# Kernel optimization log

Hardware: AMD Instinct MI355X
Metric: run time of the kernel (lower is better)

Reference implementation:

```python
import jax, jax.numpy as jnp
import numpy as np

N, E, ND, ED, HID = 50000, 400000, 128, 64, 128
GIN = 2 * ND + 2  # gnn1 input dim
CIN = 2 * HID + ED  # classifier input dim


def seg_mean(v, idx, n):
    s = jax.ops.segment_sum(v, idx, num_segments=n)
    cnt = jax.ops.segment_sum(jnp.ones((v.shape[0], 1), v.dtype), idx, num_segments=n)
    return s / jnp.maximum(cnt, 1.0)


def layer_norm(h, g, b):
    mu = h.mean(-1, keepdims=True)
    var = ((h - mu) ** 2).mean(-1, keepdims=True)
    return (h - mu) / jnp.sqrt(var + 1e-5) * g + b


def gatv2(h, src, dst, ea, wl, wr, we, att, bias, n, heads):
    # PyG GATv2Conv, concat=False, negative_slope=0.2, add_self_loops with fill_value='mean'
    C = wl.shape[1] // heads
    loop_attr = seg_mean(ea, dst, n)  # self-loop edge_attr = mean of incoming edge_attr
    ar = jnp.arange(n, dtype=src.dtype)
    s = jnp.concatenate([src, ar])
    d = jnp.concatenate([dst, ar])
    ea2 = jnp.concatenate([ea, loop_attr], axis=0)
    xl = (h @ wl).reshape(n, heads, C)
    xr = (h @ wr).reshape(n, heads, C)
    e = xl[s] + xr[d] + (ea2 @ we).reshape(-1, heads, C)  # [E2, H, C]
    e = jax.nn.leaky_relu(e, 0.2)
    logit = (e * att).sum(-1)  # [E2, H]
    m = jax.ops.segment_max(logit, d, num_segments=n)
    m = jnp.where(jnp.isfinite(m), m, 0.0)
    a = jnp.exp(logit - m[d])
    denom = jax.ops.segment_sum(a, d, num_segments=n)
    a = a / jnp.maximum(denom[d], 1e-16)
    out = jax.ops.segment_sum(xl[s] * a[..., None], d, num_segments=n)  # [N, H, C]
    return out.mean(axis=1) + bias


def setup_inputs() -> dict:
    key = jax.random.key(0)
    ks = jax.random.split(key, 32)
    w = lambda k, sh: jax.random.normal(k, sh, jnp.float32) * 0.05
    x = jax.random.normal(ks[0], (N, ND), jnp.float32)
    node_stats = jax.random.uniform(ks[1], (N, 2), jnp.float32)
    src = jax.random.randint(ks[2], (E,), 0, N)
    dst = (src + 1 + jax.random.randint(ks[3], (E,), 0, N - 1)) % N  # guarantees src != dst
    edge_index = jnp.stack([src, dst]).astype(jnp.int32)
    edge_attr = jax.random.normal(ks[4], (E, ED), jnp.float32)
    return {
        'x': x, 'node_stats': node_stats, 'edge_index': edge_index, 'edge_attr': edge_attr,
        'epw': w(ks[5], (ED, ND)), 'epb': jnp.zeros((ND,), jnp.float32),
        'g1wl': w(ks[6], (GIN, 2 * HID)), 'g1wr': w(ks[7], (GIN, 2 * HID)),
        'g1we': w(ks[8], (ED, 2 * HID)), 'g1att': w(ks[9], (2, HID)), 'g1b': jnp.zeros((HID,), jnp.float32),
        'n1g': jnp.ones((HID,), jnp.float32), 'n1b': jnp.zeros((HID,), jnp.float32),
        'g2wl': w(ks[10], (HID, HID)), 'g2wr': w(ks[11], (HID, HID)),
        'g2we': w(ks[12], (ED, HID)), 'g2att': w(ks[13], (1, HID)), 'g2b': jnp.zeros((HID,), jnp.float32),
        'n2g': jnp.ones((HID,), jnp.float32), 'n2b': jnp.zeros((HID,), jnp.float32),
        'c1w': w(ks[14], (CIN, HID)), 'c1b': jnp.zeros((HID,), jnp.float32),
        'c2w': w(ks[15], (HID, HID // 2)), 'c2b': jnp.zeros((HID // 2,), jnp.float32),
        'c3w': w(ks[16], (HID // 2, 1)), 'c3b': jnp.zeros((1,), jnp.float32),
    }


def reference(x, node_stats, edge_index, edge_attr, epw, epb, g1wl, g1wr, g1we, g1att, g1b,
              n1g, n1b, g2wl, g2wr, g2we, g2att, g2b, n2g, n2b, c1w, c1b, c2w, c2b, c3w, c3b):
    src, dst = edge_index[0], edge_index[1]
    n = x.shape[0]
    emb = jax.nn.relu(edge_attr @ epw + epb)  # [E, ND]
    x_out = seg_mean(emb, src, n)
    x_in = seg_mean(emb, dst, n)
    xi = jnp.concatenate([x_out, x_in, node_stats], axis=1)  # [N, GIN]
    h1 = jax.nn.elu(layer_norm(gatv2(xi, src, dst, edge_attr, g1wl, g1wr, g1we, g1att, g1b, n, 2), n1g, n1b))
    h2 = jax.nn.elu(layer_norm(gatv2(h1, src, dst, edge_attr, g2wl, g2wr, g2we, g2att, g2b, n, 1), n2g, n2b))
    er = jnp.concatenate([h2[src], h2[dst], edge_attr], axis=1)  # [E, CIN]
    h = jax.nn.relu(er @ c1w + c1b)
    h = jax.nn.relu(h @ c2w + c2b)
    return h @ c3w + c3b  # [E, 1]
```

## Files before the change

kernel.cpp:

```cpp
#include <hip/hip_runtime.h>
#include <cstdint>
#include <cstddef>


static inline int cdiv(int a, int b) { return (a + b - 1) / b; }

typedef __attribute__((ext_vector_type(8))) short bfrag;
typedef __attribute__((ext_vector_type(4))) float ffrag;

__device__ __forceinline__ float bf2f(unsigned short u) {
  return __uint_as_float(((unsigned)u) << 16);
}
__device__ __forceinline__ unsigned short f2bf(float f) {
  unsigned b = __float_as_uint(f);
  return (unsigned short)((b + 0x7FFFu + ((b >> 16) & 1u)) >> 16);
}

struct PrepJobs {
  const float* src[11];
  unsigned short* dst[11];
  int K[11], Nc[11], KC[11], ld[11];
};
__global__ void prep_bt(PrepJobs J) {
  int j = blockIdx.x;
  int K = J.K[j], Nc = J.Nc[j], KC = J.KC[j], ld = J.ld[j];
  const float* S = J.src[j];
  unsigned short* D = J.dst[j];
  for (int n = blockIdx.y; n < Nc; n += gridDim.y)
    for (int t = threadIdx.x; t < KC; t += blockDim.x) {
      float v = (t < K) ? S[(size_t)t * ld + n] : 0.f;
      D[(size_t)n * KC + t] = f2bf(v);
    }
}

__global__ __launch_bounds__(256) void cvt_bf16(const float* __restrict__ in,
                                                unsigned short* __restrict__ out,
                                                int n4) {
  for (int i = blockIdx.x * blockDim.x + threadIdx.x; i < n4;
       i += gridDim.x * blockDim.x) {
    float4 v = ((const float4*)in)[i];
    ((ushort4*)out)[i] = make_ushort4(f2bf(v.x), f2bf(v.y), f2bf(v.z), f2bf(v.w));
  }
}

__global__ void count_deg(const int* __restrict__ src, const int* __restrict__ dst,
                          int* __restrict__ dsrc, int* __restrict__ ddst, int E) {
  int t = blockIdx.x * blockDim.x + threadIdx.x;
  if (t < E) {
    atomicAdd(&dsrc[src[t]], 1);
    atomicAdd(&ddst[dst[t]], 1);
  }
}

__global__ __launch_bounds__(256) void scan_local(
    const int* __restrict__ degA, const int* __restrict__ degB,
    int* __restrict__ rowA, int* __restrict__ rowB, int* __restrict__ bsum,
    int N, int nb) {
  __shared__ int s[256];
  int arr = blockIdx.y;
  const int* deg = arr ? degB : degA;
  int* row = arr ? rowB : rowA;
  int b = blockIdx.x;
  int i = b * 256 + threadIdx.x;
  int v = (i < N) ? deg[i] : 0;
  s[threadIdx.x] = v;
  __syncthreads();
  for (int off = 1; off < 256; off <<= 1) {
    int t = (threadIdx.x >= off) ? s[threadIdx.x - off] : 0;
    __syncthreads();
    s[threadIdx.x] += t;
    __syncthreads();
  }
  int incl = s[threadIdx.x];
  if (i < N) row[i] = incl - v;
  if (threadIdx.x == 255) bsum[arr * nb + b] = incl;
}

__global__ __launch_bounds__(1024) void scan_bsums(int* __restrict__ bsum, int nb,
                                                   int* __restrict__ rowA,
                                                   int* __restrict__ rowB, int N) {
  __shared__ int s[1024];
  int tid = threadIdx.x;
  for (int arr = 0; arr < 2; arr++) {
    int v = (tid < nb) ? bsum[arr * nb + tid] : 0;
    s[tid] = v;
    __syncthreads();
    for (int off = 1; off < 1024; off <<= 1) {
      int t = (tid >= off) ? s[tid - off] : 0;
      __syncthreads();
      s[tid] += t;
      __syncthreads();
    }
    if (tid < nb) bsum[arr * nb + tid] = s[tid] - v;
    if (tid == nb - 1) {
      int* row = arr ? rowB : rowA;
      row[N] = s[tid];
    }
    __syncthreads();
  }
}

__global__ void scan_add(int* __restrict__ rowA, int* __restrict__ rowB,
                         int* __restrict__ curA, const int* __restrict__ bsum,
                         int N, int nb) {
  int arr = blockIdx.y;
  int* row = arr ? rowB : rowA;
  int b = blockIdx.x;
  int i = b * 256 + threadIdx.x;
  if (i < N) {
    int v = row[i] + bsum[arr * nb + b];
    row[i] = v;
    if (arr == 0) curA[i] = v;
  }
}

__global__ void ext_fix(const int* __restrict__ row_dst, int* __restrict__ row_ext,
                        int* __restrict__ cur_ext, int* __restrict__ ext_eid,
                        int E, int N) {
  int i = blockIdx.x * blockDim.x + threadIdx.x;
  if (i <= N) row_ext[i] = row_dst[i] + i;
  if (i < N) {
    cur_ext[i] = row_dst[i] + i;
    ext_eid[row_dst[i + 1] + i] = E + i;
  }
}

__global__ void scatter_eid(const int* __restrict__ src, const int* __restrict__ dst,
                            int* __restrict__ csrc, int* __restrict__ cext,
                            int* __restrict__ esrc, int* __restrict__ ext_eid,
                            int E) {
  int t = blockIdx.x * blockDim.x + threadIdx.x;
  if (t < E) {
    int p = atomicAdd(&csrc[src[t]], 1);
    esrc[p] = t;
    int q = atomicAdd(&cext[dst[t]], 1);
    ext_eid[q] = t;
  }
}

struct ASrc {
  const float *p0, *p1, *p2;
  int ld0, ld1, ld2, k0, k1;
};
__device__ __forceinline__ float loadA(const ASrc& a, int m, int k) {
  if (k < a.k0) return a.p0[(size_t)m * a.ld0 + k];
  if (k < a.k1) return a.p1[(size_t)m * a.ld1 + (k - a.k0)];
  return a.p2[(size_t)m * a.ld2 + (k - a.k1)];
}
__device__ __forceinline__ int regionOf(const ASrc& a, int k) {
  return k < a.k0 ? 0 : (k < a.k1 ? 1 : 2);
}

template <int ACT, int OBF, int ABF>
__global__ __launch_bounds__(256) void gemm_mfma(
    ASrc A, const unsigned short* __restrict__ Abf, int lda,
    const unsigned short* __restrict__ Bt, int ldbt,
    const float* __restrict__ bias, void* __restrict__ Cv, int ldc, int M, int K) {
  __shared__ __align__(16) unsigned short asb[64 * 72];
  __shared__ __align__(16) unsigned short bsb[128 * 72];
  int tid = threadIdx.x;
  int m0 = blockIdx.x * 64, n0 = blockIdx.y * 128;
  int lane = tid & 63, wave = tid >> 6;
  int quad = lane >> 4, l16 = lane & 15;
  ffrag zero = {0.f, 0.f, 0.f, 0.f};
  ffrag acc[8];
#pragma unroll
  for (int t = 0; t < 8; t++) acc[t] = zero;
  int KC = (K + 63) & ~63;
  for (int kc = 0; kc < KC; kc += 64) {
    __syncthreads();
    {
      int row = tid & 63, kq = tid >> 6;
      int gm = m0 + row;
      if (ABF) {
        const unsigned short* rp = Abf + (size_t)gm * lda + kc + kq * 16;
        ushort4 z = make_ushort4(0, 0, 0, 0);
#pragma unroll
        for (int q = 0; q < 4; q++) {
          ushort4 v = (gm < M) ? *(const ushort4*)(rp + q * 4) : z;
          *(ushort4*)&asb[row * 72 + kq * 16 + q * 4] = v;
        }
      } else {
        bool fastc = (kc + 64 <= K) && (regionOf(A, kc) == regionOf(A, kc + 63)) &&
                     (gm < M);
        if (fastc) {
          int r = regionOf(A, kc);
          const float* p;
          int ld, koff;
          if (r == 0) { p = A.p0; ld = A.ld0; koff = 0; }
          else if (r == 1) { p = A.p1; ld = A.ld1; koff = A.k0; }
          else { p = A.p2; ld = A.ld2; koff = A.k1; }
          const float* rp = p + (size_t)gm * ld + (kc - koff) + kq * 16;
#pragma unroll
          for (int q = 0; q < 4; q++) {
            float4 v = *(const float4*)(rp + q * 4);
            *(ushort4*)&asb[row * 72 + kq * 16 + q * 4] =
                make_ushort4(f2bf(v.x), f2bf(v.y), f2bf(v.z), f2bf(v.w));
          }
        } else {
#pragma unroll
          for (int q = 0; q < 16; q++) {
            int kk = kc + kq * 16 + q;
            float v = (gm < M && kk < K) ? loadA(A, gm, kk) : 0.f;
            asb[row * 72 + kq * 16 + q] = f2bf(v);
          }
        }
      }
    }
    {
      int n = tid >> 1, hf = tid & 1;
      const ushort4* rp = (const ushort4*)(Bt + (size_t)(n0 + n) * ldbt + kc + hf * 32);
      ushort4* dp = (ushort4*)&bsb[n * 72 + hf * 32];
#pragma unroll
      for (int i = 0; i < 8; i++) dp[i] = rp[i];
    }
    __syncthreads();
    int arow = wave * 16 + l16;
    bfrag a0 = *(const bfrag*)&asb[arow * 72 + quad * 8];
    bfrag a1 = *(const bfrag*)&asb[arow * 72 + 32 + quad * 8];
#pragma unroll
    for (int t = 0; t < 8; t++) {
      int bn = t * 16 + l16;
      bfrag b0 = *(const bfrag*)&bsb[bn * 72 + quad * 8];
      bfrag b1 = *(const bfrag*)&bsb[bn * 72 + 32 + quad * 8];
      acc[t] = __builtin_amdgcn_mfma_f32_16x16x32_bf16(a0, b0, acc[t], 0, 0, 0);
      acc[t] = __builtin_amdgcn_mfma_f32_16x16x32_bf16(a1, b1, acc[t], 0, 0, 0);
    }
  }
#pragma unroll
  for (int t = 0; t < 8; t++) {
    int col = n0 + t * 16 + l16;
    float bv = bias ? bias[col] : 0.f;
#pragma unroll
    for (int r = 0; r < 4; r++) {
      int row = m0 + wave * 16 + quad * 4 + r;
      if (row < M) {
        float v = acc[t][r] + bv;
        if (ACT == 1) v = fmaxf(v, 0.f);
        if (OBF)
          ((unsigned short*)Cv)[(size_t)row * ldc + col] = f2bf(v);
        else
          ((float*)Cv)[(size_t)row * ldc + col] = v;
      }
    }
  }
}

__global__ __launch_bounds__(256) void gather_mean(
    const int* __restrict__ row_src, const int* __restrict__ eid_src,
    const int* __restrict__ row_ext, const int* __restrict__ ext_eid,
    const unsigned short* __restrict__ emb, const unsigned short* __restrict__ eab,
    float* __restrict__ xout, float* __restrict__ xin,
    unsigned short* __restrict__ lattrb, int N) {
  int lane = threadIdx.x & 63, wid = threadIdx.x >> 6;
  int n = blockIdx.x * 4 + wid;
  int side = blockIdx.y;
  if (n >= N) return;
  int lo, hi;
  const int* eid;
  if (side) { lo = row_ext[n]; hi = row_ext[n + 1] - 1; eid = ext_eid; }
  else { lo = row_src[n]; hi = row_src[n + 1]; eid = eid_src; }
  float a0 = 0.f, a1 = 0.f, la = 0.f;
  for (int j = lo; j < hi; j++) {
    int e = eid[j];
    ushort2 v = *(const ushort2*)&emb[(size_t)e * 128 + lane * 2];
    a0 += bf2f(v.x);
    a1 += bf2f(v.y);
    if (side) la += bf2f(eab[(size_t)e * 64 + lane]);
  }
  float r = 1.f / fmaxf((float)(hi - lo), 1.f);
  float* ob = side ? xin : xout;
  *(float2*)&ob[(size_t)n * 128 + lane * 2] = make_float2(a0 * r, a1 * r);
  if (side) lattrb[(size_t)n * 64 + lane] = f2bf(la * r);
}

template <int H>
__global__ __launch_bounds__(256) void attn_logits_mfma(
    const unsigned short* __restrict__ xl, const unsigned short* __restrict__ xr,
    const int* __restrict__ src, const int* __restrict__ dst,
    const unsigned short* __restrict__ eab, const unsigned short* __restrict__ lattrb,
    const int* __restrict__ ext_eid,
    const unsigned short* __restrict__ wet, const float* __restrict__ att,
    float* __restrict__ lg, int E, int N) {
  constexpr int HC = H * 128;
  __shared__ __align__(16) unsigned short asb[64 * 72];
  __shared__ __align__(16) unsigned short bsb[128 * 72];
  __shared__ float atts[128];
  __shared__ int sidx[64], didx[64];
  unsigned short* Cs = bsb;
  int tid = threadIdx.x;
  int E2 = E + N;
  int i0 = blockIdx.x * 64;
  int lane = tid & 63, wave = tid >> 6, quad = lane >> 4, l16 = lane & 15;
  if (tid < 64) {
    int j = i0 + tid;
    int s = 0, d = 0;
    if (j < E2) {
      int e = ext_eid[j];
      if (e < E) { s = src[e]; d = dst[e]; }
      else { s = d = e - E; }
    }
    sidx[tid] = s;
    didx[tid] = d;
  }
  {
    int row = tid & 63, kq = tid >> 6;
    int j = i0 + row;
    if (j < E2) {
      int e = ext_eid[j];
      const unsigned short* ap =
          (e < E) ? eab + (size_t)e * 64 : lattrb + (size_t)(e - E) * 64;
      const ushort4* rp = (const ushort4*)(ap + kq * 16);
#pragma unroll
      for (int q = 0; q < 4; q++)
        *(ushort4*)&asb[row * 72 + kq * 16 + q * 4] = rp[q];
    } else {
      ushort4 z = make_ushort4(0, 0, 0, 0);
#pragma unroll
      for (int q = 0; q < 4; q++) *(ushort4*)&asb[row * 72 + kq * 16 + q * 4] = z;
    }
  }
  int er = tid >> 4, cc = tid & 15;
  ffrag zero = {0.f, 0.f, 0.f, 0.f};
  for (int head = 0; head < H; head++) {
    int n0 = head * 128;
    __syncthreads();
    if (tid < 128) atts[tid] = att[n0 + tid];
    {
      int n = tid >> 1, hf = tid & 1;
      const ushort4* rp = (const ushort4*)(wet + (size_t)(n0 + n) * 64 + hf * 32);
      ushort4* dp = (ushort4*)&bsb[n * 72 + hf * 32];
#pragma unroll
      for (int i = 0; i < 8; i++) dp[i] = rp[i];
    }
    __syncthreads();
    int arow = wave * 16 + l16;
    bfrag a0 = *(const bfrag*)&asb[arow * 72 + quad * 8];
    bfrag a1 = *(const bfrag*)&asb[arow * 72 + 32 + quad * 8];
    ffrag acc[8];
#pragma unroll
    for (int t = 0; t < 8; t++) {
      acc[t] = zero;
      int bn = t * 16 + l16;
      bfrag b0 = *(const bfrag*)&bsb[bn * 72 + quad * 8];
      bfrag b1 = *(const bfrag*)&bsb[bn * 72 + 32 + quad * 8];
      acc[t] = __builtin_amdgcn_mfma_f32_16x16x32_bf16(a0, b0, acc[t], 0, 0, 0);
      acc[t] = __builtin_amdgcn_mfma_f32_16x16x32_bf16(a1, b1, acc[t], 0, 0, 0);
    }
    __syncthreads();
    {
      int rb = wave * 16 + quad * 4;
#pragma unroll
      for (int t = 0; t < 8; t++)
#pragma unroll
        for (int r = 0; r < 4; r++)
          Cs[(rb + r) * 136 + t * 16 + l16] = f2bf(acc[t][r]);
    }
    __syncthreads();
#pragma unroll
    for (int i2 = 0; i2 < 4; i2++) {
      int r = er * 4 + i2;
      int gi = i0 + r;
      float ps = 0.f;
      if (gi < E2) {
        int s = sidx[r], d = didx[r];
#pragma unroll
        for (int h = 0; h < 2; h++) {
          int c = h * 64 + cc * 4;
          ushort4 mv = *(const ushort4*)&Cs[r * 136 + c];
          ushort4 xlu = *(const ushort4*)&xl[(size_t)s * HC + n0 + c];
          ushort4 xru = *(const ushort4*)&xr[(size_t)d * HC + n0 + c];
          float e0 = bf2f(mv.x) + bf2f(xlu.x) + bf2f(xru.x);
          float e1 = bf2f(mv.y) + bf2f(xlu.y) + bf2f(xru.y);
          float e2 = bf2f(mv.z) + bf2f(xlu.z) + bf2f(xru.z);
          float e3 = bf2f(mv.w) + bf2f(xlu.w) + bf2f(xru.w);
          e0 = e0 > 0.f ? e0 : 0.2f * e0;
          e1 = e1 > 0.f ? e1 : 0.2f * e1;
          e2 = e2 > 0.f ? e2 : 0.2f * e2;
          e3 = e3 > 0.f ? e3 : 0.2f * e3;
          ps += e0 * atts[c + 0] + e1 * atts[c + 1] + e2 * atts[c + 2] +
                e3 * atts[c + 3];
        }
      }
      ps += __shfl_xor(ps, 1);
      ps += __shfl_xor(ps, 2);
      ps += __shfl_xor(ps, 4);
      ps += __shfl_xor(ps, 8);
      if (cc == 0 && gi < E2) lg[(size_t)gi * H + head] = ps;
    }
  }
}

template <int H>
__global__ __launch_bounds__(256) void attn_fused(
    const unsigned short* __restrict__ xl, const float* __restrict__ lg,
    const int* __restrict__ row_ext, const int* __restrict__ ext_eid,
    const int* __restrict__ src, const float* __restrict__ bias,
    const float* __restrict__ gam, const float* __restrict__ bet,
    unsigned short* __restrict__ hout, int E, int N) {
  constexpr int HC = H * 128;
  constexpr int CPL = HC / 64;
  int lane = threadIdx.x & 63, wid = threadIdx.x >> 6;
  int n = blockIdx.x * 4 + wid;
  if (n >= N) return;
  int lo = row_ext[n], hi = row_ext[n + 1];
  int myh = (H == 2) ? (lane >> 5) : 0;
  int colbase = (H == 2) ? (myh * 128 + (lane & 31) * 4) : (lane * 2);
  float m = -3.4e38f;
  for (int j = lo; j < hi; j++) m = fmaxf(m, lg[(size_t)j * H + myh]);
  float asum = 0.f;
  float acc[CPL] = {};
  for (int j = lo; j < hi; j++) {
    int e = ext_eid[j];
    int s = (e < E) ? src[e] : (e - E);
    float a = __expf(lg[(size_t)j * H + myh] - m);
    asum += a;
    const unsigned short* xp = &xl[(size_t)s * HC + colbase];
    if (H == 2) {
      ushort4 u = *(const ushort4*)xp;
      acc[0] += a * bf2f(u.x);
      acc[1] += a * bf2f(u.y);
      acc[2] += a * bf2f(u.z);
      acc[3] += a * bf2f(u.w);
    } else {
      ushort2 u = *(const ushort2*)xp;
      acc[0] += a * bf2f(u.x);
      acc[1] += a * bf2f(u.y);
    }
  }
  float inv = 1.f / fmaxf(asum, 1e-16f);
#pragma unroll
  for (int k = 0; k < CPL; k++) acc[k] *= inv;
  int ch;
  if (H == 2) {
#pragma unroll
    for (int k = 0; k < CPL; k++) acc[k] = (acc[k] + __shfl_xor(acc[k], 32)) * 0.5f;
    ch = (lane & 31) * CPL;
  } else {
    ch = lane * CPL;
  }
#pragma unroll
  for (int k = 0; k < CPL; k++) acc[k] += bias[ch + k];
  float s = 0.f;
#pragma unroll
  for (int k = 0; k < CPL; k++) s += acc[k];
#pragma unroll
  for (int mm = 1; mm < 64; mm <<= 1) s += __shfl_xor(s, mm);
  constexpr float dupn = (H == 2) ? 256.f : 128.f;
  float mu = s / dupn;
  float vs = 0.f;
#pragma unroll
  for (int k = 0; k < CPL; k++) {
    acc[k] -= mu;
    vs += acc[k] * acc[k];
  }
#pragma unroll
  for (int mm = 1; mm < 64; mm <<= 1) vs += __shfl_xor(vs, mm);
  float rstd = rsqrtf(vs / dupn + 1e-5f);
  float y[CPL];
#pragma unroll
  for (int k = 0; k < CPL; k++) {
    float v = acc[k] * rstd * gam[ch + k] + bet[ch + k];
    y[k] = v > 0.f ? v : expm1f(v);
  }
  if (H == 2) {
    if (lane < 32)
      *(ushort4*)&hout[(size_t)n * 128 + ch] =
          make_ushort4(f2bf(y[0]), f2bf(y[1]), f2bf(y[2]), f2bf(y[3]));
  } else {
    *(ushort2*)&hout[(size_t)n * 128 + ch] = make_ushort2(f2bf(y[0]), f2bf(y[1]));
  }
}

__global__ __launch_bounds__(256) void classifier_mfma(
    const unsigned short* __restrict__ eab, const unsigned short* __restrict__ Wct,
    const int* __restrict__ eid_src,
    const int* __restrict__ src, const int* __restrict__ dst,
    const float* __restrict__ P, const float* __restrict__ Q,
    const float* __restrict__ c1b, const unsigned short* __restrict__ c2t,
    const float* __restrict__ c2b, const float* __restrict__ c3w,
    const float* __restrict__ c3b, float* __restrict__ out, int E) {
  __shared__ __align__(16) unsigned short asb[64 * 72];
  __shared__ __align__(16) unsigned short bsb[128 * 72];
  __shared__ __align__(16) unsigned short t1s[64 * 136];
  __shared__ float c1bs[128];
  __shared__ float c2bs[64], c3ws[64];
  __shared__ int sidx[64], didx[64], eidx[64];
  int tid = threadIdx.x;
  int e0 = blockIdx.x * 64;
  int lane = tid & 63, wave = tid >> 6, quad = lane >> 4, l16 = lane & 15;
  if (tid < 128) c1bs[tid] = c1b[tid];
  if (tid < 64) {
    c2bs[tid] = c2b[tid];
    c3ws[tid] = c3w[tid];
    int j = e0 + tid;
    int e = (j < E) ? eid_src[j] : 0;
    eidx[tid] = (j < E) ? e : -1;
    sidx[tid] = src[e];
    didx[tid] = dst[e];
  }
  {
    int row = tid & 63, kq = tid >> 6;
    int j = e0 + row;
    if (j < E) {
      int e = eid_src[j];
      const ushort4* rp = (const ushort4*)(eab + (size_t)e * 64 + kq * 16);
#pragma unroll
      for (int q = 0; q < 4; q++)
        *(ushort4*)&asb[row * 72 + kq * 16 + q * 4] = rp[q];
    } else {
      ushort4 z = make_ushort4(0, 0, 0, 0);
#pragma unroll
      for (int q = 0; q < 4; q++) *(ushort4*)&asb[row * 72 + kq * 16 + q * 4] = z;
    }
  }
  {
    int n = tid >> 1, hf = tid & 1;
    const ushort4* rp = (const ushort4*)(Wct + (size_t)n * 64 + hf * 32);
    ushort4* dp = (ushort4*)&bsb[n * 72 + hf * 32];
#pragma unroll
    for (int i = 0; i < 8; i++) dp[i] = rp[i];
  }
  __syncthreads();
  ffrag zero = {0.f, 0.f, 0.f, 0.f};
  int arow = wave * 16 + l16;
  {
    bfrag a0 = *(const bfrag*)&asb[arow * 72 + quad * 8];
    bfrag a1 = *(const bfrag*)&asb[arow * 72 + 32 + quad * 8];
    ffrag acc[8];
#pragma unroll
    for (int t = 0; t < 8; t++) {
      acc[t] = zero;
      int bn = t * 16 + l16;
      bfrag b0 = *(const bfrag*)&bsb[bn * 72 + quad * 8];
      bfrag b1 = *(const bfrag*)&bsb[bn * 72 + 32 + quad * 8];
      acc[t] = __builtin_amdgcn_mfma_f32_16x16x32_bf16(a0, b0, acc[t], 0, 0, 0);
      acc[t] = __builtin_amdgcn_mfma_f32_16x16x32_bf16(a1, b1, acc[t], 0, 0, 0);
    }
    __syncthreads();
    int rb = wave * 16 + quad * 4;
#pragma unroll
    for (int t = 0; t < 8; t++)
#pragma unroll
      for (int r = 0; r < 4; r++)
        t1s[(rb + r) * 136 + t * 16 + l16] = f2bf(acc[t][r]);
  }
  __syncthreads();
  {
    int erow = tid >> 4, ccc = tid & 15;
#pragma unroll
    for (int i2 = 0; i2 < 4; i2++) {
      int r = erow * 4 + i2;
      int s = sidx[r], d = didx[r];
#pragma unroll
      for (int h = 0; h < 2; h++) {
        int c = h * 64 + ccc * 4;
        ushort4 mv = *(const ushort4*)&t1s[r * 136 + c];
        float4 pv = *(const float4*)&P[(size_t)s * 128 + c];
        float4 qv = *(const float4*)&Q[(size_t)d * 128 + c];
        float v0 = fmaxf(bf2f(mv.x) + pv.x + qv.x + c1bs[c + 0], 0.f);
        float v1 = fmaxf(bf2f(mv.y) + pv.y + qv.y + c1bs[c + 1], 0.f);
        float v2 = fmaxf(bf2f(mv.z) + pv.z + qv.z + c1bs[c + 2], 0.f);
        float v3 = fmaxf(bf2f(mv.w) + pv.w + qv.w + c1bs[c + 3], 0.f);
        *(ushort4*)&t1s[r * 136 + c] =
            make_ushort4(f2bf(v0), f2bf(v1), f2bf(v2), f2bf(v3));
      }
    }
    int n = tid >> 2, qq = tid & 3;
    const ushort4* rp = (const ushort4*)(c2t + (size_t)n * 128 + qq * 32);
    ushort4* dp = (ushort4*)&bsb[n * 136 + qq * 32];
#pragma unroll
    for (int i = 0; i < 8; i++) dp[i] = rp[i];
  }
  __syncthreads();
  {
    bfrag pa[4];
#pragma unroll
    for (int kc = 0; kc < 4; kc++)
      pa[kc] = *(const bfrag*)&t1s[arow * 136 + kc * 32 + quad * 8];
    ffrag acc2[4];
#pragma unroll
    for (int t = 0; t < 4; t++) {
      acc2[t] = zero;
      int bn = t * 16 + l16;
#pragma unroll
      for (int kc = 0; kc < 4; kc++) {
        bfrag b = *(const bfrag*)&bsb[bn * 136 + kc * 32 + quad * 8];
        acc2[t] = __builtin_amdgcn_mfma_f32_16x16x32_bf16(pa[kc], b, acc2[t], 0, 0, 0);
      }
    }
    float c3b0 = c3b[0];
    float rsum[4] = {0.f, 0.f, 0.f, 0.f};
#pragma unroll
    for (int t = 0; t < 4; t++) {
      int col = t * 16 + l16;
      float cb = c2bs[col], cw = c3ws[col];
#pragma unroll
      for (int r = 0; r < 4; r++)
        rsum[r] += fmaxf(acc2[t][r] + cb, 0.f) * cw;
    }
#pragma unroll
    for (int r = 0; r < 4; r++) {
      rsum[r] += __shfl_xor(rsum[r], 1);
      rsum[r] += __shfl_xor(rsum[r], 2);
      rsum[r] += __shfl_xor(rsum[r], 4);
      rsum[r] += __shfl_xor(rsum[r], 8);
    }
    if (l16 == 0) {
#pragma unroll
      for (int r = 0; r < 4; r++) {
        int e = eidx[wave * 16 + quad * 4 + r];
        if (e >= 0) out[e] = rsum[r] + c3b0;
      }
    }
  }
}

extern "C" void kernel_launch(void* const* d_in, const int* in_sizes, int n_in,
                              void* d_out, int out_size, void* d_ws, size_t ws_size,
                              hipStream_t stream) {
  const int N = in_sizes[1] / 2;
  const int E = in_sizes[3] / 64;
  const int E2 = E + N;
  const int nb = cdiv(N, 256);

  const float* node_stats = (const float*)d_in[1];
  const int* src = (const int*)d_in[2];
  const int* dst = (const int*)d_in[2] + E;
  const float* edge_attr = (const float*)d_in[3];
  const float* epw = (const float*)d_in[4];
  const float* epb = (const float*)d_in[5];
  const float* g1wl = (const float*)d_in[6];
  const float* g1wr = (const float*)d_in[7];
  const float* g1we = (const float*)d_in[8];
  const float* g1att = (const float*)d_in[9];
  const float* g1b = (const float*)d_in[10];
  const float* n1g = (const float*)d_in[11];
  const float* n1b = (const float*)d_in[12];
  const float* g2wl = (const float*)d_in[13];
  const float* g2wr = (const float*)d_in[14];
  const float* g2we = (const float*)d_in[15];
  const float* g2att = (const float*)d_in[16];
  const float* g2b = (const float*)d_in[17];
  const float* n2g = (const float*)d_in[18];
  const float* n2b = (const float*)d_in[19];
  const float* c1w = (const float*)d_in[20];
  const float* c1b = (const float*)d_in[21];
  const float* c2w = (const float*)d_in[22];
  const float* c2b = (const float*)d_in[23];
  const float* c3w = (const float*)d_in[24];
  const float* c3b = (const float*)d_in[25];
  float* out = (float*)d_out;

  float* w = (float*)d_ws;
  size_t o = 0;
  auto alloc = [&](size_t n) { float* p = w + o; o += n; return p; };
  float* xout = alloc((size_t)N * 128);
  float* xin = alloc((size_t)N * 128);
  float* lattr = alloc((size_t)N * 64);
  float* lg = alloc((size_t)E2 * 2);
  int* row_src = (int*)alloc((size_t)(N + 1));
  int* row_dst = (int*)alloc((size_t)(N + 1));
  int* row_ext = (int*)alloc((size_t)(N + 1));
  int* deg_src = (int*)alloc((size_t)N);
  int* deg_dst = (int*)alloc((size_t)N);
  int* cur_src = (int*)alloc((size_t)N);
  int* cur_ext = (int*)alloc((size_t)N);
  int* eid_src = (int*)alloc((size_t)E);
  int* ext_eid = (int*)alloc((size_t)E2);
  int* bsum = (int*)alloc((size_t)2 * 1024);
  unsigned short* wb = (unsigned short*)alloc(140000);
  unsigned short* eab = (unsigned short*)alloc((size_t)E * 32);
  float* R = alloc((size_t)E * 64);
  unsigned short* Ru = (unsigned short*)R;
  unsigned short* emb = Ru;
  unsigned short* xl1b = Ru;
  unsigned short* xr1b = Ru + (size_t)N * 256;
  unsigned short* h1b = Ru + (size_t)N * 512;
  unsigned short* xl2b = Ru + (size_t)N * 640;
  unsigned short* xr2b = Ru + (size_t)N * 768;
  unsigned short* h2b = Ru + (size_t)N * 896;
  unsigned short* lattrb = (unsigned short*)lattr;
  float* P = xout;
  float* Q = xin;

  unsigned short* epwt = wb + 0;
  unsigned short* g1wlt = wb + 8192;
  unsigned short* g1wrt = wb + 90112;
  unsigned short* g1wet = wb + 172032;
  unsigned short* g2wlt = wb + 188416;
  unsigned short* g2wrt = wb + 204800;
  unsigned short* g2wet = wb + 221184;
  unsigned short* c1wat = wb + 229376;
  unsigned short* c1wbt = wb + 245760;
  unsigned short* c1wct = wb + 262144;
  unsigned short* c2t = wb + 270336;

  cvt_bf16<<<2048, 256, 0, stream>>>(edge_attr, eab, E * 16);
  PrepJobs J;
  auto setj = [&](int i, const float* s, unsigned short* d2, int K, int Nc,
                  int KC, int ld) {
    J.src[i] = s; J.dst[i] = d2; J.K[i] = K; J.Nc[i] = Nc; J.KC[i] = KC; J.ld[i] = ld;
  };
  setj(0, epw, epwt, 64, 128, 64, 128);
  setj(1, g1wl, g1wlt, 258, 256, 320, 256);
  setj(2, g1wr, g1wrt, 258, 256, 320, 256);
  setj(3, g1we, g1wet, 64, 256, 64, 256);
  setj(4, g2wl, g2wlt, 128, 128, 128, 128);
  setj(5, g2wr, g2wrt, 128, 128, 128, 128);
  setj(6, g2we, g2wet, 64, 128, 64, 128);
  setj(7, c1w, c1wat, 128, 128, 128, 128);
  setj(8, c1w + 128 * 128, c1wbt, 128, 128, 128, 128);
  setj(9, c1w + 256 * 128, c1wct, 64, 128, 64, 128);
  setj(10, c2w, c2t, 128, 64, 128, 64);
  prep_bt<<<dim3(11, 32), 256, 0, stream>>>(J);

  hipMemsetAsync(deg_src, 0, (size_t)2 * N * sizeof(int), stream);
  count_deg<<<cdiv(E, 256), 256, 0, stream>>>(src, dst, deg_src, deg_dst, E);
  scan_local<<<dim3(nb, 2), 256, 0, stream>>>(deg_src, deg_dst, row_src, row_dst,
                                              bsum, N, nb);
  scan_bsums<<<1, 1024, 0, stream>>>(bsum, nb, row_src, row_dst, N);
  scan_add<<<dim3(nb, 2), 256, 0, stream>>>(row_src, row_dst, cur_src, bsum, N, nb);
  ext_fix<<<cdiv(N + 1, 256), 256, 0, stream>>>(row_dst, row_ext, cur_ext,
                                                ext_eid, E, N);
  scatter_eid<<<cdiv(E, 256), 256, 0, stream>>>(src, dst, cur_src, cur_ext,
                                                eid_src, ext_eid, E);

  ASrc dummy{nullptr, nullptr, nullptr, 0, 0, 0, 0, 0};

  gemm_mfma<1, 1, 1><<<dim3(cdiv(E, 64), 1), 256, 0, stream>>>(
      dummy, eab, 64, epwt, 64, epb, emb, 128, E, 64);
  gather_mean<<<dim3(cdiv(N, 4), 2), 256, 0, stream>>>(
      row_src, eid_src, row_ext, ext_eid, emb, eab, xout, xin, lattrb, N);

  {
    ASrc a{xout, xin, node_stats, 128, 128, 2, 128, 256};
    dim3 g(cdiv(N, 64), 2);
    gemm_mfma<0, 1, 0><<<g, 256, 0, stream>>>(a, nullptr, 0, g1wlt, 320, nullptr,
                                              xl1b, 256, N, 258);
    gemm_mfma<0, 1, 0><<<g, 256, 0, stream>>>(a, nullptr, 0, g1wrt, 320, nullptr,
                                              xr1b, 256, N, 258);
  }

  attn_logits_mfma<2><<<cdiv(E2, 64), 256, 0, stream>>>(
      xl1b, xr1b, src, dst, eab, lattrb, ext_eid, g1wet, g1att, lg, E, N);
  attn_fused<2><<<cdiv(N, 4), 256, 0, stream>>>(xl1b, lg, row_ext, ext_eid, src,
                                                g1b, n1g, n1b, h1b, E, N);

  {
    dim3 g(cdiv(N, 64), 1);
    gemm_mfma<0, 1, 1><<<g, 256, 0, stream>>>(dummy, h1b, 128, g2wlt, 128,
                                              nullptr, xl2b, 128, N, 128);
    gemm_mfma<0, 1, 1><<<g, 256, 0, stream>>>(dummy, h1b, 128, g2wrt, 128,
                                              nullptr, xr2b, 128, N, 128);
  }

  attn_logits_mfma<1><<<cdiv(E2, 64), 256, 0, stream>>>(
      xl2b, xr2b, src, dst, eab, lattrb, ext_eid, g2wet, g2att, lg, E, N);
  attn_fused<1><<<cdiv(N, 4), 256, 0, stream>>>(xl2b, lg, row_ext, ext_eid, src,
                                                g2b, n2g, n2b, h2b, E, N);

  {
    dim3 g(cdiv(N, 64), 1);
    gemm_mfma<0, 0, 1><<<g, 256, 0, stream>>>(dummy, h2b, 128, c1wat, 128,
                                              nullptr, P, 128, N, 128);
    gemm_mfma<0, 0, 1><<<g, 256, 0, stream>>>(dummy, h2b, 128, c1wbt, 128,
                                              nullptr, Q, 128, N, 128);
  }
  classifier_mfma<<<cdiv(E, 64), 256, 0, stream>>>(
      eab, c1wct, eid_src, src, dst, P, Q, c1b, c2t, c2b, c3w, c3b, out, E);
}
```

Before: 1.035 ms.

## Fuse edge embedding GEMM with segment-mean scatter and gather h2 in classifier

The separate edge-embedding GEMM and the gather_mean kernel are replaced by an emb_mean kernel. It computes relu(edge_attr@epw+epb) per 64 sorted edges in MFMA and run-length atomically adds the rows into per-node sums, so the E×128 emb buffer is never written or read back. Division by degree moves into the A-loader of the first GNN GEMM, and the loop-attribute mean gets a small normalize kernel. The classifier drops the precomputed P/Q node GEMMs and instead gathers h2[src] and h2[dst] rows, running the full K=320 first layer per edge. This trades redundant per-edge FLOPs and atomics for less memory traffic and fewer launches.

```diff
diff --git a/kernel.cpp b/kernel.cpp
--- a/kernel.cpp
+++ b/kernel.cpp
@@ -140,11 +140,20 @@
 
 struct ASrc {
   const float *p0, *p1, *p2;
+  const int *s0, *s1;
   int ld0, ld1, ld2, k0, k1;
 };
 __device__ __forceinline__ float loadA(const ASrc& a, int m, int k) {
-  if (k < a.k0) return a.p0[(size_t)m * a.ld0 + k];
-  if (k < a.k1) return a.p1[(size_t)m * a.ld1 + (k - a.k0)];
+  if (k < a.k0) {
+    float v = a.p0[(size_t)m * a.ld0 + k];
+    if (a.s0) v *= 1.f / fmaxf((float)a.s0[m], 1.f);
+    return v;
+  }
+  if (k < a.k1) {
+    float v = a.p1[(size_t)m * a.ld1 + (k - a.k0)];
+    if (a.s1) v *= 1.f / fmaxf((float)a.s1[m], 1.f);
+    return v;
+  }
   return a.p2[(size_t)m * a.ld2 + (k - a.k1)];
 }
 __device__ __forceinline__ int regionOf(const ASrc& a, int k) {
@@ -186,16 +195,19 @@
         if (fastc) {
           int r = regionOf(A, kc);
           const float* p;
+          const int* sp;
           int ld, koff;
-          if (r == 0) { p = A.p0; ld = A.ld0; koff = 0; }
-          else if (r == 1) { p = A.p1; ld = A.ld1; koff = A.k0; }
-          else { p = A.p2; ld = A.ld2; koff = A.k1; }
+          if (r == 0) { p = A.p0; ld = A.ld0; koff = 0; sp = A.s0; }
+          else if (r == 1) { p = A.p1; ld = A.ld1; koff = A.k0; sp = A.s1; }
+          else { p = A.p2; ld = A.ld2; koff = A.k1; sp = nullptr; }
+          float sc = sp ? 1.f / fmaxf((float)sp[gm], 1.f) : 1.f;
           const float* rp = p + (size_t)gm * ld + (kc - koff) + kq * 16;
 #pragma unroll
           for (int q = 0; q < 4; q++) {
             float4 v = *(const float4*)(rp + q * 4);
             *(ushort4*)&asb[row * 72 + kq * 16 + q * 4] =
-                make_ushort4(f2bf(v.x), f2bf(v.y), f2bf(v.z), f2bf(v.w));
+                make_ushort4(f2bf(v.x * sc), f2bf(v.y * sc), f2bf(v.z * sc),
+                             f2bf(v.w * sc));
           }
         } else {
 #pragma unroll
@@ -246,32 +258,117 @@
   }
 }
 
-__global__ __launch_bounds__(256) void gather_mean(
-    const int* __restrict__ row_src, const int* __restrict__ eid_src,
-    const int* __restrict__ row_ext, const int* __restrict__ ext_eid,
-    const unsigned short* __restrict__ emb, const unsigned short* __restrict__ eab,
-    float* __restrict__ xout, float* __restrict__ xin,
-    unsigned short* __restrict__ lattrb, int N) {
-  int lane = threadIdx.x & 63, wid = threadIdx.x >> 6;
-  int n = blockIdx.x * 4 + wid;
-  int side = blockIdx.y;
-  if (n >= N) return;
-  int lo, hi;
-  const int* eid;
-  if (side) { lo = row_ext[n]; hi = row_ext[n + 1] - 1; eid = ext_eid; }
-  else { lo = row_src[n]; hi = row_src[n + 1]; eid = eid_src; }
-  float a0 = 0.f, a1 = 0.f, la = 0.f;
-  for (int j = lo; j < hi; j++) {
-    int e = eid[j];
-    ushort2 v = *(const ushort2*)&emb[(size_t)e * 128 + lane * 2];
-    a0 += bf2f(v.x);
-    a1 += bf2f(v.y);
-    if (side) la += bf2f(eab[(size_t)e * 64 + lane]);
-  }
-  float r = 1.f / fmaxf((float)(hi - lo), 1.f);
-  float* ob = side ? xin : xout;
-  *(float2*)&ob[(size_t)n * 128 + lane * 2] = make_float2(a0 * r, a1 * r);
-  if (side) lattrb[(size_t)n * 64 + lane] = f2bf(la * r);
+template <int EXT>
+__global__ __launch_bounds__(256) void emb_mean(
+    const unsigned short* __restrict__ eab, const int* __restrict__ eid,
+    const int* __restrict__ nidarr, const unsigned short* __restrict__ epwt,
+    const float* __restrict__ epb, float* __restrict__ xsum,
+    float* __restrict__ lsum, int NE, int E) {
+  __shared__ __align__(16) unsigned short asb[64 * 72];
+  __shared__ __align__(16) unsigned short bsb[128 * 72];
+  __shared__ float Cs[64 * 132];
+  __shared__ int nids[64];
+  __shared__ float epbs[128];
+  int tid = threadIdx.x;
+  int i0 = blockIdx.x * 64;
+  int lane = tid & 63, wave = tid >> 6, quad = lane >> 4, l16 = lane & 15;
+  if (tid < 128) epbs[tid] = epb[tid];
+  if (tid < 64) {
+    int j = i0 + tid, nid = -1;
+    if (j < NE) {
+      int e = eid[j];
+      if (e < E) nid = nidarr[e];
+    }
+    nids[tid] = nid;
+  }
+  {
+    int row = tid & 63, kq = tid >> 6;
+    int j = i0 + row;
+    int e = (j < NE) ? eid[j] : E;
+    if (e < E) {
+      const ushort4* rp = (const ushort4*)(eab + (size_t)e * 64 + kq * 16);
+#pragma unroll
+      for (int q = 0; q < 4; q++)
+        *(ushort4*)&asb[row * 72 + kq * 16 + q * 4] = rp[q];
+    } else {
+      ushort4 z = make_ushort4(0, 0, 0, 0);
+#pragma unroll
+      for (int q = 0; q < 4; q++) *(ushort4*)&asb[row * 72 + kq * 16 + q * 4] = z;
+    }
+  }
+  {
+    int n = tid >> 1, hf = tid & 1;
+    const ushort4* rp = (const ushort4*)(epwt + (size_t)n * 64 + hf * 32);
+    ushort4* dp = (ushort4*)&bsb[n * 72 + hf * 32];
+#pragma unroll
+    for (int i = 0; i < 8; i++) dp[i] = rp[i];
+  }
+  __syncthreads();
+  ffrag zero = {0.f, 0.f, 0.f, 0.f};
+  int arow = wave * 16 + l16;
+  bfrag a0 = *(const bfrag*)&asb[arow * 72 + quad * 8];
+  bfrag a1 = *(const bfrag*)&asb[arow * 72 + 32 + quad * 8];
+  ffrag acc[8];
+#pragma unroll
+  for (int t = 0; t < 8; t++) {
+    acc[t] = zero;
+    int bn = t * 16 + l16;
+    bfrag b0 = *(const bfrag*)&bsb[bn * 72 + quad * 8];
+    bfrag b1 = *(const bfrag*)&bsb[bn * 72 + 32 + quad * 8];
+    acc[t] = __builtin_amdgcn_mfma_f32_16x16x32_bf16(a0, b0, acc[t], 0, 0, 0);
+    acc[t] = __builtin_amdgcn_mfma_f32_16x16x32_bf16(a1, b1, acc[t], 0, 0, 0);
+  }
+  {
+    int rb = wave * 16 + quad * 4;
+#pragma unroll
+    for (int t = 0; t < 8; t++) {
+      int col = t * 16 + l16;
+#pragma unroll
+      for (int r = 0; r < 4; r++)
+        Cs[(rb + r) * 132 + col] = fmaxf(acc[t][r] + epbs[col], 0.f);
+    }
+  }
+  __syncthreads();
+  {
+    int c = tid & 127, half = tid >> 7;
+    float run = 0.f;
+    int cur = -1;
+    for (int r = half * 32; r < half * 32 + 32; r++) {
+      int n = nids[r];
+      if (n != cur) {
+        if (cur >= 0) atomicAdd(&xsum[(size_t)cur * 128 + c], run);
+        run = 0.f;
+        cur = n;
+      }
+      if (n >= 0) run += Cs[r * 132 + c];
+    }
+    if (cur >= 0) atomicAdd(&xsum[(size_t)cur * 128 + c], run);
+  }
+  if (EXT) {
+    int c = tid & 63, grp = tid >> 6;
+    float run = 0.f;
+    int cur = -1;
+    for (int r = grp * 16; r < grp * 16 + 16; r++) {
+      int n = nids[r];
+      if (n != cur) {
+        if (cur >= 0) atomicAdd(&lsum[(size_t)cur * 64 + c], run);
+        run = 0.f;
+        cur = n;
+      }
+      if (n >= 0) run += bf2f(asb[r * 72 + c]);
+    }
+    if (cur >= 0) atomicAdd(&lsum[(size_t)cur * 64 + c], run);
+  }
+}
+
+__global__ void norm_lattr(const float* __restrict__ ls,
+                           const int* __restrict__ degd,
+                           unsigned short* __restrict__ lb, int N) {
+  int i = blockIdx.x * blockDim.x + threadIdx.x;
+  if (i < N * 64) {
+    int n = i >> 6;
+    lb[i] = f2bf(ls[i] / fmaxf((float)degd[n], 1.f));
+  }
 }
 
 template <int H>
@@ -473,14 +570,15 @@
 }
 
 __global__ __launch_bounds__(256) void classifier_mfma(
-    const unsigned short* __restrict__ eab, const unsigned short* __restrict__ Wct,
+    const unsigned short* __restrict__ eab, const unsigned short* __restrict__ h2b,
     const int* __restrict__ eid_src,
     const int* __restrict__ src, const int* __restrict__ dst,
-    const float* __restrict__ P, const float* __restrict__ Q,
+    const unsigned short* __restrict__ c1wct, const unsigned short* __restrict__ c1wat,
+    const unsigned short* __restrict__ c1wbt,
     const float* __restrict__ c1b, const unsigned short* __restrict__ c2t,
     const float* __restrict__ c2b, const float* __restrict__ c3w,
     const float* __restrict__ c3b, float* __restrict__ out, int E) {
-  __shared__ __align__(16) unsigned short asb[64 * 72];
+  __shared__ __align__(16) unsigned short asb[64 * 136];
   __shared__ __align__(16) unsigned short bsb[128 * 72];
   __shared__ __align__(16) unsigned short t1s[64 * 136];
   __shared__ float c1bs[128];
@@ -494,76 +592,94 @@
     c2bs[tid] = c2b[tid];
     c3ws[tid] = c3w[tid];
     int j = e0 + tid;
-    int e = (j < E) ? eid_src[j] : 0;
-    eidx[tid] = (j < E) ? e : -1;
-    sidx[tid] = src[e];
-    didx[tid] = dst[e];
-  }
+    int e = (j < E) ? eid_src[j] : -1;
+    eidx[tid] = e;
+    sidx[tid] = (e >= 0) ? src[e] : 0;
+    didx[tid] = (e >= 0) ? dst[e] : 0;
+  }
+  __syncthreads();
+  ffrag zero = {0.f, 0.f, 0.f, 0.f};
+  ffrag acc[8];
+#pragma unroll
+  for (int t = 0; t < 8; t++) acc[t] = zero;
+  int arow = wave * 16 + l16;
   {
     int row = tid & 63, kq = tid >> 6;
-    int j = e0 + row;
-    if (j < E) {
-      int e = eid_src[j];
+    int e = eidx[row];
+    if (e >= 0) {
       const ushort4* rp = (const ushort4*)(eab + (size_t)e * 64 + kq * 16);
 #pragma unroll
       for (int q = 0; q < 4; q++)
-        *(ushort4*)&asb[row * 72 + kq * 16 + q * 4] = rp[q];
+        *(ushort4*)&asb[row * 136 + kq * 16 + q * 4] = rp[q];
     } else {
       ushort4 z = make_ushort4(0, 0, 0, 0);
 #pragma unroll
-      for (int q = 0; q < 4; q++) *(ushort4*)&asb[row * 72 + kq * 16 + q * 4] = z;
-    }
-  }
-  {
+      for (int q = 0; q < 4; q++) *(ushort4*)&asb[row * 136 + kq * 16 + q * 4] = z;
+    }
     int n = tid >> 1, hf = tid & 1;
-    const ushort4* rp = (const ushort4*)(Wct + (size_t)n * 64 + hf * 32);
+    const ushort4* rp2 = (const ushort4*)(c1wct + (size_t)n * 64 + hf * 32);
     ushort4* dp = (ushort4*)&bsb[n * 72 + hf * 32];
 #pragma unroll
-    for (int i = 0; i < 8; i++) dp[i] = rp[i];
+    for (int i = 0; i < 8; i++) dp[i] = rp2[i];
   }
   __syncthreads();
-  ffrag zero = {0.f, 0.f, 0.f, 0.f};
-  int arow = wave * 16 + l16;
-  {
-    bfrag a0 = *(const bfrag*)&asb[arow * 72 + quad * 8];
-    bfrag a1 = *(const bfrag*)&asb[arow * 72 + 32 + quad * 8];
-    ffrag acc[8];
+  {
+    bfrag a0 = *(const bfrag*)&asb[arow * 136 + quad * 8];
+    bfrag a1 = *(const bfrag*)&asb[arow * 136 + 32 + quad * 8];
 #pragma unroll
     for (int t = 0; t < 8; t++) {
-      acc[t] = zero;
       int bn = t * 16 + l16;
       bfrag b0 = *(const bfrag*)&bsb[bn * 72 + quad * 8];
       bfrag b1 = *(const bfrag*)&bsb[bn * 72 + 32 + quad * 8];
       acc[t] = __builtin_amdgcn_mfma_f32_16x16x32_bf16(a0, b0, acc[t], 0, 0, 0);
       acc[t] = __builtin_amdgcn_mfma_f32_16x16x32_bf16(a1, b1, acc[t], 0, 0, 0);
     }
-    __syncthreads();
+  }
+  for (int ph = 0; ph < 2; ph++) {
+    const int* idx = ph ? didx : sidx;
+    const unsigned short* Wt = ph ? c1wbt : c1wat;
+    __syncthreads();
+    {
+      int row = tid & 63, kq = tid >> 6;
+      int s = idx[row];
+      const ushort4* rp = (const ushort4*)(h2b + (size_t)s * 128 + kq * 32);
+      ushort4* dp = (ushort4*)&asb[row * 136 + kq * 32];
+#pragma unroll
+      for (int i = 0; i < 8; i++) dp[i] = rp[i];
+    }
+#pragma unroll
+    for (int kc = 0; kc < 2; kc++) {
+      if (kc) __syncthreads();
+      {
+        int n = tid >> 1, hf = tid & 1;
+        const ushort4* rp = (const ushort4*)(Wt + (size_t)n * 128 + kc * 64 + hf * 32);
+        ushort4* dp = (ushort4*)&bsb[n * 72 + hf * 32];
+#pragma unroll
+        for (int i = 0; i < 8; i++) dp[i] = rp[i];
+      }
+      __syncthreads();
+      bfrag a0 = *(const bfrag*)&asb[arow * 136 + kc * 64 + quad * 8];
+      bfrag a1 = *(const bfrag*)&asb[arow * 136 + kc * 64 + 32 + quad * 8];
+#pragma unroll
+      for (int t = 0; t < 8; t++) {
+        int bn = t * 16 + l16;
+        bfrag b0 = *(const bfrag*)&bsb[bn * 72 + quad * 8];
+        bfrag b1 = *(const bfrag*)&bsb[bn * 72 + 32 + quad * 8];
+        acc[t] = __builtin_amdgcn_mfma_f32_16x16x32_bf16(a0, b0, acc[t], 0, 0, 0);
+        acc[t] = __builtin_amdgcn_mfma_f32_16x16x32_bf16(a1, b1, acc[t], 0, 0, 0);
+      }
+    }
+  }
+  __syncthreads();
+  {
     int rb = wave * 16 + quad * 4;
 #pragma unroll
-    for (int t = 0; t < 8; t++)
-#pragma unroll
-      for (int r = 0; r < 4; r++)
-        t1s[(rb + r) * 136 + t * 16 + l16] = f2bf(acc[t][r]);
-  }
-  __syncthreads();
-  {
-    int erow = tid >> 4, ccc = tid & 15;
-#pragma unroll
-    for (int i2 = 0; i2 < 4; i2++) {
-      int r = erow * 4 + i2;
-      int s = sidx[r], d = didx[r];
-#pragma unroll
-      for (int h = 0; h < 2; h++) {
-        int c = h * 64 + ccc * 4;
-        ushort4 mv = *(const ushort4*)&t1s[r * 136 + c];
-        float4 pv = *(const float4*)&P[(size_t)s * 128 + c];
-        float4 qv = *(const float4*)&Q[(size_t)d * 128 + c];
-        float v0 = fmaxf(bf2f(mv.x) + pv.x + qv.x + c1bs[c + 0], 0.f);
-        float v1 = fmaxf(bf2f(mv.y) + pv.y + qv.y + c1bs[c + 1], 0.f);
-        float v2 = fmaxf(bf2f(mv.z) + pv.z + qv.z + c1bs[c + 2], 0.f);
-        float v3 = fmaxf(bf2f(mv.w) + pv.w + qv.w + c1bs[c + 3], 0.f);
-        *(ushort4*)&t1s[r * 136 + c] =
-            make_ushort4(f2bf(v0), f2bf(v1), f2bf(v2), f2bf(v3));
+    for (int t = 0; t < 8; t++) {
+      int col = t * 16 + l16;
+#pragma unroll
+      for (int r = 0; r < 4; r++) {
+        float v = acc[t][r] + c1bs[col];
+        t1s[(rb + r) * 136 + col] = f2bf(fmaxf(v, 0.f));
       }
     }
     int n = tid >> 2, qq = tid & 3;
@@ -657,7 +773,8 @@
   auto alloc = [&](size_t n) { float* p = w + o; o += n; return p; };
   float* xout = alloc((size_t)N * 128);
   float* xin = alloc((size_t)N * 128);
-  float* lattr = alloc((size_t)N * 64);
+  float* lattr_sum = alloc((size_t)N * 64);
+  unsigned short* lattrb = (unsigned short*)alloc((size_t)N * 32);
   float* lg = alloc((size_t)E2 * 2);
   int* row_src = (int*)alloc((size_t)(N + 1));
   int* row_dst = (int*)alloc((size_t)(N + 1));
@@ -671,18 +788,14 @@
   int* bsum = (int*)alloc((size_t)2 * 1024);
   unsigned short* wb = (unsigned short*)alloc(140000);
   unsigned short* eab = (unsigned short*)alloc((size_t)E * 32);
-  float* R = alloc((size_t)E * 64);
+  float* R = alloc((size_t)N * 512);
   unsigned short* Ru = (unsigned short*)R;
-  unsigned short* emb = Ru;
   unsigned short* xl1b = Ru;
   unsigned short* xr1b = Ru + (size_t)N * 256;
   unsigned short* h1b = Ru + (size_t)N * 512;
   unsigned short* xl2b = Ru + (size_t)N * 640;
   unsigned short* xr2b = Ru + (size_t)N * 768;
   unsigned short* h2b = Ru + (size_t)N * 896;
-  unsigned short* lattrb = (unsigned short*)lattr;
-  float* P = xout;
-  float* Q = xin;
 
   unsigned short* epwt = wb + 0;
   unsigned short* g1wlt = wb + 8192;
@@ -714,6 +827,7 @@
   setj(9, c1w + 256 * 128, c1wct, 64, 128, 64, 128);
   setj(10, c2w, c2t, 128, 64, 128, 64);
   prep_bt<<<dim3(11, 32), 256, 0, stream>>>(J);
+  hipMemsetAsync(xout, 0, (size_t)N * 320 * sizeof(float), stream);
 
   hipMemsetAsync(deg_src, 0, (size_t)2 * N * sizeof(int), stream);
   count_deg<<<cdiv(E, 256), 256, 0, stream>>>(src, dst, deg_src, deg_dst, E);
@@ -726,15 +840,16 @@
   scatter_eid<<<cdiv(E, 256), 256, 0, stream>>>(src, dst, cur_src, cur_ext,
                                                 eid_src, ext_eid, E);
 
-  ASrc dummy{nullptr, nullptr, nullptr, 0, 0, 0, 0, 0};
-
-  gemm_mfma<1, 1, 1><<<dim3(cdiv(E, 64), 1), 256, 0, stream>>>(
-      dummy, eab, 64, epwt, 64, epb, emb, 128, E, 64);
-  gather_mean<<<dim3(cdiv(N, 4), 2), 256, 0, stream>>>(
-      row_src, eid_src, row_ext, ext_eid, emb, eab, xout, xin, lattrb, N);
-
-  {
-    ASrc a{xout, xin, node_stats, 128, 128, 2, 128, 256};
+  ASrc dummy{nullptr, nullptr, nullptr, nullptr, nullptr, 0, 0, 0, 0, 0};
+
+  emb_mean<0><<<cdiv(E, 64), 256, 0, stream>>>(eab, eid_src, src, epwt, epb,
+                                               xout, nullptr, E, E);
+  emb_mean<1><<<cdiv(E2, 64), 256, 0, stream>>>(eab, ext_eid, dst, epwt, epb,
+                                                xin, lattr_sum, E2, E);
+  norm_lattr<<<cdiv(N * 64, 256), 256, 0, stream>>>(lattr_sum, deg_dst, lattrb, N);
+
+  {
+    ASrc a{xout, xin, node_stats, deg_src, deg_dst, 128, 128, 2, 128, 256};
     dim3 g(cdiv(N, 64), 2);
     gemm_mfma<0, 1, 0><<<g, 256, 0, stream>>>(a, nullptr, 0, g1wlt, 320, nullptr,
                                               xl1b, 256, N, 258);
@@ -760,13 +875,7 @@
   attn_fused<1><<<cdiv(N, 4), 256, 0, stream>>>(xl2b, lg, row_ext, ext_eid, src,
                                                 g2b, n2g, n2b, h2b, E, N);
 
-  {
-    dim3 g(cdiv(N, 64), 1);
-    gemm_mfma<0, 0, 1><<<g, 256, 0, stream>>>(dummy, h2b, 128, c1wat, 128,
-                                              nullptr, P, 128, N, 128);
-    gemm_mfma<0, 0, 1><<<g, 256, 0, stream>>>(dummy, h2b, 128, c1wbt, 128,
-                                              nullptr, Q, 128, N, 128);
-  }
   classifier_mfma<<<cdiv(E, 64), 256, 0, stream>>>(
-      eab, c1wct, eid_src, src, dst, P, Q, c1b, c2t, c2b, c3w, c3b, out, E);
-}
+      eab, h2b, eid_src, src, dst, c1wct, c1wat, c1wbt, c1b, c2t, c2b, c3w,
+      c3b, out, E);
+}
```

New measurement: 1.110 ms. 7.2% more time.
